# Kernel tuning notes

Hardware: AMD Instinct MI355X
Metric: run time of the kernel (lower is better)

The kernel has to match this reference:

```python
import jax, jax.numpy as jnp
import numpy as np

N_NODES = 50000
N_EDGES = 800000
IN_DIM = 128
HID_DIM = 64
OUT_DIM = 40
N_REL = 8


def setup_inputs() -> dict:
    key = jax.random.key(0)
    ks = jax.random.split(key, 12)
    x = jax.random.normal(ks[0], (N_NODES, IN_DIM), dtype=jnp.float32)
    edge_index = jax.random.randint(ks[1], (2, N_EDGES), 0, N_NODES, dtype=jnp.int64)
    edge_type = jax.random.randint(ks[2], (N_EDGES,), 0, N_REL, dtype=jnp.int64)
    s = 0.05
    W1 = jax.random.normal(ks[3], (N_REL, IN_DIM, HID_DIM), dtype=jnp.float32) * s
    root1 = jax.random.normal(ks[4], (IN_DIM, HID_DIM), dtype=jnp.float32) * s
    b1 = jnp.zeros((HID_DIM,), dtype=jnp.float32)
    W2 = jax.random.normal(ks[5], (N_REL, HID_DIM, HID_DIM), dtype=jnp.float32) * s
    root2 = jax.random.normal(ks[6], (HID_DIM, HID_DIM), dtype=jnp.float32) * s
    b2 = jnp.zeros((HID_DIM,), dtype=jnp.float32)
    Wl = jax.random.normal(ks[7], (HID_DIM, OUT_DIM), dtype=jnp.float32) * s
    bl = jnp.zeros((OUT_DIM,), dtype=jnp.float32)
    return {"x": x, "edge_index": edge_index, "edge_type": edge_type,
            "W1": W1, "root1": root1, "b1": b1,
            "W2": W2, "root2": root2, "b2": b2,
            "Wl": Wl, "bl": bl}


def _rgcn_conv(x, W, Wroot, b, src, dst, edge_type):
    # PyG RGCNConv (no bases/blocks, aggr='mean'):
    #   out[i] = sum_r mean_{(j->i) of rel r} (x[j] @ W[r]) + x[i] @ Wroot + b
    N = x.shape[0]
    R = W.shape[0]
    h = jnp.einsum('ni,rio->rno', x, W)        # [R, N, out]
    msgs = h[edge_type, src]                   # [E, out] edge gather
    seg = edge_type * N + dst                  # per (relation, dst) segment
    sums = jax.ops.segment_sum(msgs, seg, num_segments=R * N)
    cnt = jax.ops.segment_sum(jnp.ones((msgs.shape[0],), x.dtype), seg,
                              num_segments=R * N)
    mean = sums / jnp.maximum(cnt, 1.0)[:, None]
    agg = mean.reshape(R, N, -1).sum(axis=0)   # sum over relations
    return agg + x @ Wroot + b


def reference(x, edge_index, edge_type, W1, root1, b1, W2, root2, b2, Wl, bl):
    src, dst = edge_index[0], edge_index[1]
    h = jax.nn.relu(_rgcn_conv(x, W1, root1, b1, src, dst, edge_type))
    # dropout is identity in eval mode
    h = jax.nn.relu(_rgcn_conv(h, W2, root2, b2, src, dst, edge_type))
    logits = h @ Wl + bl
    return jax.nn.log_softmax(logits, axis=1)
```

## Files before the change

### kernel.cpp

```cpp
#include <hip/hip_runtime.h>
#include <hip/hip_bf16.h>
#include <cmath>


#define IN_DIM 128
#define HID 64
#define OUT_DIM 40
#define NREL 8
#define NCOLS 576
#define K2 576
#define CAPR 32
#define EVR 256
#define CSTR 16

typedef __attribute__((ext_vector_type(8))) short short8;
typedef __attribute__((ext_vector_type(4))) short short4v;
typedef __attribute__((ext_vector_type(4))) float floatx4;

static __device__ __forceinline__ short f2bf(float f) {
  __hip_bfloat16 h = __float2bfloat16(f);
  return __builtin_bit_cast(short, h);
}
static __device__ __forceinline__ float bflo(unsigned int u) {
  return __int_as_float(u << 16);
}
static __device__ __forceinline__ float bfhi(unsigned int u) {
  return __int_as_float(u & 0xffff0000u);
}
static __device__ __forceinline__ unsigned int packbf(float x, float y) {
  unsigned int lo = (unsigned short)f2bf(x);
  unsigned int hi = (unsigned short)f2bf(y);
  return lo | (hi << 16);
}
static __device__ __forceinline__ float bf2f(short s) {
  return __int_as_float(((unsigned int)(unsigned short)s) << 16);
}

__global__ void pack_bt(const float* __restrict__ W1, const float* __restrict__ root1,
                        short* __restrict__ Bt1,
                        const float* __restrict__ W2, const float* __restrict__ root2,
                        short* __restrict__ Bt2b,
                        const float* __restrict__ Wl, short* __restrict__ WlB,
                        int* __restrict__ cursor, int nzero4) {
  const int PB1 = (NCOLS * IN_DIM + 255) / 256;
  const int PB2 = (64 * K2 + 255) / 256;
  const int PBW = (96 * HID + 255) / 256;
  int b = blockIdx.x;
  if (b < PB1) {
    int i = b * 256 + threadIdx.x;
    if (i >= NCOLS * IN_DIM) return;
    int c = i / IN_DIM, k = i % IN_DIM;
    float v = (c < NREL * HID)
      ? W1[((size_t)(c >> 6) * IN_DIM + k) * HID + (c & 63)]
      : root1[(size_t)k * HID + (c - NREL * HID)];
    Bt1[i] = f2bf(v);
  } else if (b < PB1 + PB2) {
    int i = (b - PB1) * 256 + threadIdx.x;
    if (i >= 64 * K2) return;
    int col = i / K2, kk = i % K2;
    float v = (kk < NREL * HID)
      ? W2[(size_t)kk * HID + col]
      : root2[(size_t)(kk - NREL * HID) * HID + col];
    Bt2b[i] = f2bf(v);
  } else if (b < PB1 + PB2 + PBW) {
    int i = (b - PB1 - PB2) * 256 + threadIdx.x;
    if (i >= 96 * HID) return;
    int row = i / HID, k = i % HID;
    int c = row % 48;
    float v = (c < OUT_DIM) ? Wl[(size_t)k * OUT_DIM + c] : 0.f;
    short hi = f2bf(v);
    if (row < 48) WlB[i] = hi;
    else          WlB[i] = f2bf(v - bf2f(hi));
  } else {
    int i = (b - PB1 - PB2 - PBW) * 256 + threadIdx.x;
    if (i < nzero4) {
      int4 z; z.x = 0; z.y = 0; z.z = 0; z.w = 0;
      ((int4*)cursor)[i] = z;
    }
  }
}

__device__ __forceinline__ void gemm1_body(
    short* As, short* Bs,
    const float* __restrict__ A, const short* __restrict__ Bt,
    const float* __restrict__ bias, short* __restrict__ H,
    unsigned short* __restrict__ AGG, int M, int row0)
{
  constexpr int K = IN_DIM;
  constexpr int AST = K + 8;
  int tid = threadIdx.x;
  int wv = tid >> 6, lane = tid & 63;
  int lm = lane & 15, quad = lane >> 4;

  {
    constexpr int CH = K / 4;
    for (int i = tid; i < 64 * CH; i += 256) {
      int r = i / CH, kq = i % CH;
      int gr = row0 + r; if (gr >= M) gr = M - 1;
      float4 v = *(const float4*)(A + (unsigned)(gr * K + kq * 4));
      short4v s;
      s.x = f2bf(v.x); s.y = f2bf(v.y); s.z = f2bf(v.z); s.w = f2bf(v.w);
      *(short4v*)(As + r * AST + kq * 4) = s;
    }
  }

  const short* ap = As + (16 * wv + lm) * AST + quad * 8;

  for (int cy = 0; cy < 9; ++cy) {
    constexpr int CB = K / 8;
    for (int i = tid; i < 64 * CB; i += 256) {
      int n = i / CB, ko = i % CB;
      short8 v = *(const short8*)(Bt + (unsigned)((cy * 64 + n) * K + ko * 8));
      *(short8*)(Bs + n * AST + ko * 8) = v;
    }
    __syncthreads();

    floatx4 acc[4] = {{0,0,0,0},{0,0,0,0},{0,0,0,0},{0,0,0,0}};
    #pragma unroll
    for (int ks = 0; ks < K / 32; ++ks) {
      short8 a = *(const short8*)(ap + ks * 32);
      #pragma unroll
      for (int nb = 0; nb < 4; ++nb) {
        short8 b = *(const short8*)(Bs + (nb * 16 + lm) * AST + ks * 32 + quad * 8);
        acc[nb] = __builtin_amdgcn_mfma_f32_16x16x32_bf16(a, b, acc[nb], 0, 0, 0);
      }
    }
    __syncthreads();

    int mbase = row0 + 16 * wv + quad * 4;
    if (cy < 8) {
      #pragma unroll
      for (int nb = 0; nb < 4; ++nb) {
        int col = cy * 64 + nb * 16 + lm;
        #pragma unroll
        for (int r = 0; r < 4; ++r) {
          int mg = mbase + r;
          if (mg < M) H[(unsigned)mg * (NREL * HID) + col] = f2bf(acc[nb][r]);
        }
      }
    } else {
      #pragma unroll
      for (int nb = 0; nb < 4; ++nb) {
        int col = nb * 16 + lm;
        float bv = bias[col];
        #pragma unroll
        for (int r = 0; r < 4; ++r) {
          int mg = mbase + r;
          if (mg < M)
            AGG[(unsigned)mg * HID + col] = (unsigned short)f2bf(acc[nb][r] + bv);
        }
      }
    }
  }
}

__global__ __launch_bounds__(256, 4) void gemm1_scatter(
    const float* __restrict__ A, const short* __restrict__ Bt,
    const float* __restrict__ bias, short* __restrict__ H,
    unsigned short* __restrict__ AGG, int M, int GB,
    const int* __restrict__ src, const int* __restrict__ dst,
    const int* __restrict__ et,
    int* __restrict__ cursor, int* __restrict__ ev, int E)
{
  constexpr int AST = IN_DIM + 8;
  __shared__ short As[64 * AST];
  __shared__ short Bs[64 * AST];
  if ((int)blockIdx.x < GB) {
    gemm1_body(As, Bs, A, Bt, bias, H, AGG, M, blockIdx.x * 64);
  } else {
    int e = (blockIdx.x - GB) * 256 + threadIdx.x;
    if (e >= E) return;
    int d = dst[e];
    int r = et[e];
    int pos = atomicAdd(&cursor[d * CSTR + r], 1);
    if (pos < CAPR)
      __builtin_nontemporal_store(src[e], &ev[(d << 8) + (r << 5) + pos]);
  }
}

__global__ __launch_bounds__(256) void csr_agg1(
    const short* __restrict__ H1, const int* __restrict__ cursor,
    const int* __restrict__ ev, unsigned short* __restrict__ h, int N)
{
  int tid = threadIdx.x;
  int wv = tid >> 6, lane = tid & 63;
  int rel = lane >> 3, dg = lane & 7;
  int d = blockIdx.x * 4 + wv;

  int cnt = cursor[d * CSTR + rel]; if (cnt > CAPR) cnt = CAPR;
  const int* evg = ev + ((size_t)d << 8) + (rel << 5);
  int evs = evg[dg];

  float acc[8] = {0.f,0.f,0.f,0.f,0.f,0.f,0.f,0.f};
  for (int s = 0; s < cnt; ++s) {
    int srcj = (s < 8) ? __shfl(evs, (lane & 56) + s, 64) : evg[s];
    uint4 hv = *(const uint4*)(H1 + ((size_t)srcj << 9) + (rel << 6) + (dg << 3));
    acc[0] += bflo(hv.x); acc[1] += bfhi(hv.x);
    acc[2] += bflo(hv.y); acc[3] += bfhi(hv.y);
    acc[4] += bflo(hv.z); acc[5] += bfhi(hv.z);
    acc[6] += bflo(hv.w); acc[7] += bfhi(hv.w);
  }
  float w = (cnt > 0) ? (1.0f / (float)cnt) : 0.0f;
  #pragma unroll
  for (int j = 0; j < 8; ++j) acc[j] *= w;
  #pragma unroll
  for (int off = 8; off <= 32; off <<= 1) {
    #pragma unroll
    for (int j = 0; j < 8; ++j) acc[j] += __shfl_xor(acc[j], off, 64);
  }
  if (rel == 0) {
    unsigned short* hrow = h + (size_t)d * HID + (dg << 3);
    uint4 sv = *(const uint4*)hrow;
    float v0 = fmaxf(acc[0] + bflo(sv.x), 0.f);
    float v1 = fmaxf(acc[1] + bfhi(sv.x), 0.f);
    float v2 = fmaxf(acc[2] + bflo(sv.y), 0.f);
    float v3 = fmaxf(acc[3] + bfhi(sv.y), 0.f);
    float v4 = fmaxf(acc[4] + bflo(sv.z), 0.f);
    float v5 = fmaxf(acc[5] + bfhi(sv.z), 0.f);
    float v6 = fmaxf(acc[6] + bflo(sv.w), 0.f);
    float v7 = fmaxf(acc[7] + bfhi(sv.w), 0.f);
    uint4 ov;
    ov.x = packbf(v0, v1); ov.y = packbf(v2, v3);
    ov.z = packbf(v4, v5); ov.w = packbf(v6, v7);
    *(uint4*)hrow = ov;
  }
}

__global__ __launch_bounds__(256) void agg2(
    const unsigned short* __restrict__ h, const int* __restrict__ cursor,
    const int* __restrict__ ev, short* __restrict__ m2, int N)
{
  int tid = threadIdx.x;
  int wv = tid >> 6, lane = tid & 63;
  int rel = lane >> 3, dg = lane & 7;
  int d = blockIdx.x * 4 + wv;

  int cnt = cursor[d * CSTR + rel]; if (cnt > CAPR) cnt = CAPR;
  const int* evg = ev + ((size_t)d << 8) + (rel << 5);
  int evs = evg[dg];

  float acc[8] = {0.f,0.f,0.f,0.f,0.f,0.f,0.f,0.f};
  for (int s = 0; s < cnt; ++s) {
    int srcj = (s < 8) ? __shfl(evs, (lane & 56) + s, 64) : evg[s];
    uint4 hv = *(const uint4*)(h + ((size_t)srcj << 6) + (dg << 3));
    acc[0] += bflo(hv.x); acc[1] += bfhi(hv.x);
    acc[2] += bflo(hv.y); acc[3] += bfhi(hv.y);
    acc[4] += bflo(hv.z); acc[5] += bfhi(hv.z);
    acc[6] += bflo(hv.w); acc[7] += bfhi(hv.w);
  }
  float w = (cnt > 0) ? (1.0f / (float)cnt) : 0.0f;
  uint4 ov;
  ov.x = packbf(acc[0] * w, acc[1] * w);
  ov.y = packbf(acc[2] * w, acc[3] * w);
  ov.z = packbf(acc[4] * w, acc[5] * w);
  ov.w = packbf(acc[6] * w, acc[7] * w);
  *(uint4*)(m2 + (size_t)d * K2 + (rel << 6) + (dg << 3)) = ov;
  if (rel == 0) {
    uint4 hv = *(const uint4*)(h + ((size_t)d << 6) + (dg << 3));
    *(uint4*)(m2 + (size_t)d * K2 + 512 + (dg << 3)) = hv;
  }
}

__global__ __launch_bounds__(256) void gemm2c(
    const short* __restrict__ m2, const short* __restrict__ Bt2b,
    const short* __restrict__ WlB, const float* __restrict__ b2,
    const float* __restrict__ bl, float* __restrict__ out, int N)
{
  constexpr int AST = 64 + 8;
  __shared__ short As[64 * AST];
  __shared__ short Bs[64 * AST];
  __shared__ short zb[64 * AST];
  __shared__ short Wb[96 * AST];
  __shared__ float sb2[64];
  __shared__ float sbl[48];
  int tid = threadIdx.x;
  int wv = tid >> 6, lane = tid & 63;
  int lm = lane & 15, quad = lane >> 4;
  int row0 = blockIdx.x * 64;

  #pragma unroll
  for (int j = 0; j < 3; ++j) {
    int i = tid + j * 256;
    int r = i >> 3, ch = i & 7;
    *(short8*)(Wb + r * AST + ch * 8) = *(const short8*)(WlB + r * 64 + ch * 8);
  }
  if (tid < 64) sb2[tid] = b2[tid];
  if (tid < 48) sbl[tid] = (tid < OUT_DIM) ? bl[tid] : 0.f;

  floatx4 acc[4] = {{0,0,0,0},{0,0,0,0},{0,0,0,0},{0,0,0,0}};
  for (int kt = 0; kt < 9; ++kt) {
    #pragma unroll
    for (int j = 0; j < 2; ++j) {
      int i = tid + j * 256;
      int r = i >> 3, ch = i & 7;
      int gr = row0 + r; if (gr >= N) gr = N - 1;
      *(short8*)(As + r * AST + ch * 8) =
          *(const short8*)(m2 + (size_t)gr * K2 + kt * 64 + ch * 8);
      *(short8*)(Bs + r * AST + ch * 8) =
          *(const short8*)(Bt2b + (unsigned)(r * K2 + kt * 64 + ch * 8));
    }
    __syncthreads();
    #pragma unroll
    for (int ks = 0; ks < 2; ++ks) {
      short8 a = *(const short8*)(As + (16 * wv + lm) * AST + ks * 32 + quad * 8);
      #pragma unroll
      for (int nb = 0; nb < 4; ++nb) {
        short8 b = *(const short8*)(Bs + (nb * 16 + lm) * AST + ks * 32 + quad * 8);
        acc[nb] = __builtin_amdgcn_mfma_f32_16x16x32_bf16(b, a, acc[nb], 0, 0, 0);
      }
    }
    __syncthreads();
  }

  int zrow = 16 * wv + lm;
  #pragma unroll
  for (int nb = 0; nb < 4; ++nb) {
    int c0 = nb * 16 + quad * 4;
    float4 bv = *(const float4*)(sb2 + c0);
    short4v s;
    s.x = f2bf(fmaxf(acc[nb][0] + bv.x, 0.f));
    s.y = f2bf(fmaxf(acc[nb][1] + bv.y, 0.f));
    s.z = f2bf(fmaxf(acc[nb][2] + bv.z, 0.f));
    s.w = f2bf(fmaxf(acc[nb][3] + bv.w, 0.f));
    *(short4v*)(zb + zrow * AST + c0) = s;
  }

  floatx4 acc2[3] = {{0,0,0,0},{0,0,0,0},{0,0,0,0}};
  #pragma unroll
  for (int ks = 0; ks < 2; ++ks) {
    short8 a = *(const short8*)(zb + zrow * AST + ks * 32 + quad * 8);
    #pragma unroll
    for (int nb2 = 0; nb2 < 3; ++nb2) {
      short8 bh = *(const short8*)(Wb + (nb2 * 16 + lm) * AST + ks * 32 + quad * 8);
      short8 bl_ = *(const short8*)(Wb + (48 + nb2 * 16 + lm) * AST + ks * 32 + quad * 8);
      acc2[nb2] = __builtin_amdgcn_mfma_f32_16x16x32_bf16(bh, a, acc2[nb2], 0, 0, 0);
      acc2[nb2] = __builtin_amdgcn_mfma_f32_16x16x32_bf16(bl_, a, acc2[nb2], 0, 0, 0);
    }
  }

  float lv[3][4];
  float m = -__builtin_inff();
  #pragma unroll
  for (int nb2 = 0; nb2 < 3; ++nb2) {
    #pragma unroll
    for (int r = 0; r < 4; ++r) {
      int col = nb2 * 16 + quad * 4 + r;
      float t = acc2[nb2][r] + sbl[col];
      lv[nb2][r] = t;
      if (col < OUT_DIM) m = fmaxf(m, t);
    }
  }
  m = fmaxf(m, __shfl_xor(m, 16, 64));
  m = fmaxf(m, __shfl_xor(m, 32, 64));
  float s = 0.f;
  #pragma unroll
  for (int nb2 = 0; nb2 < 3; ++nb2) {
    #pragma unroll
    for (int r = 0; r < 4; ++r) {
      int col = nb2 * 16 + quad * 4 + r;
      if (col < OUT_DIM) s += expf(lv[nb2][r] - m);
    }
  }
  s += __shfl_xor(s, 16, 64);
  s += __shfl_xor(s, 32, 64);
  float lg = logf(s);
  int dd = row0 + zrow;
  if (dd < N) {
    float* orow = out + (size_t)dd * OUT_DIM;
    #pragma unroll
    for (int nb2 = 0; nb2 < 3; ++nb2) {
      #pragma unroll
      for (int r = 0; r < 4; ++r) {
        int col = nb2 * 16 + quad * 4 + r;
        if (col < OUT_DIM) orow[col] = lv[nb2][r] - m - lg;
      }
    }
  }
}

extern "C" void kernel_launch(void* const* d_in, const int* in_sizes, int n_in,
                              void* d_out, int out_size, void* d_ws, size_t ws_size,
                              hipStream_t stream) {
  const float* x     = (const float*)d_in[0];
  const int*   eidx  = (const int*)d_in[1];
  const int*   etype = (const int*)d_in[2];
  const float* W1    = (const float*)d_in[3];
  const float* root1 = (const float*)d_in[4];
  const float* b1    = (const float*)d_in[5];
  const float* W2    = (const float*)d_in[6];
  const float* root2 = (const float*)d_in[7];
  const float* b2    = (const float*)d_in[8];
  const float* Wl    = (const float*)d_in[9];
  const float* bl    = (const float*)d_in[10];

  int N = in_sizes[0] / IN_DIM;
  int E = in_sizes[2];
  const int* srcp = eidx;
  const int* dstp = eidx + E;

  char* ws = (char*)d_ws;
  size_t off = 0;
  auto alloc = [&](size_t bytes) -> char* {
    char* p = ws + off;
    off += (bytes + 255) & ~(size_t)255;
    return p;
  };
  short* Bt1    = (short*)alloc((size_t)NCOLS * IN_DIM * 2);
  short* Bt2b   = (short*)alloc((size_t)64 * K2 * 2);
  short* WlB    = (short*)alloc((size_t)96 * HID * 2);
  int*   cursor = (int*)alloc((size_t)N * CSTR * 4);
  int*   ev     = (int*)alloc((size_t)N * EVR * 4);
  char*  h1m2   = alloc((size_t)N * K2 * 2);
  short* H1     = (short*)h1m2;
  short* m2     = (short*)h1m2;
  unsigned short* AGG1 = (unsigned short*)alloc((size_t)N * HID * 2);

  const int PB1 = (NCOLS * IN_DIM + 255) / 256;
  const int PB2 = (64 * K2 + 255) / 256;
  const int PBW = (96 * HID + 255) / 256;
  int nzero4 = (N * CSTR) / 4;
  int ZB = (nzero4 + 255) / 256;
  pack_bt<<<PB1 + PB2 + PBW + ZB, 256, 0, stream>>>(
      W1, root1, Bt1, W2, root2, Bt2b, Wl, WlB, cursor, nzero4);

  int GB = (N + 63) / 64;
  int SB = (E + 255) / 256;
  gemm1_scatter<<<GB + SB, 256, 0, stream>>>(x, Bt1, b1, H1, AGG1, N, GB,
                                             srcp, dstp, etype, cursor, ev, E);

  csr_agg1<<<N / 4, 256, 0, stream>>>(H1, cursor, ev, AGG1, N);

  agg2<<<N / 4, 256, 0, stream>>>(AGG1, cursor, ev, m2, N);

  gemm2c<<<GB, 256, 0, stream>>>(m2, Bt2b, WlB, b2, bl, (float*)d_out, N);
}
```

Before: 225.9 us.

## Fuse layer-2 aggregation into GEMM, compact edge buckets, relation-major H1 layout

The agg2 kernel is folded into gemm2c. Each block now gathers and means neighbour features for its 64 rows directly into a full-K shared-memory A tile, so the m2 intermediate no longer makes a round trip through global memory. Edge buckets shrink from 32 slots per relation to 8 inline slots plus a separate spill array, which cuts scatter footprint and lets one coalesced load fetch all 64 indices per node. H1 is stored relation-major and csr_agg1 is rewritten so each lane group handles one edge slot across relations with fixed unrolled loads. The trade-off is a serial spill path for high-degree buckets and much larger shared memory in gemm2c, which may lower occupancy.

Result: slower. 298.8 us (+32.3%).

```diff
diff --git a/kernel.cpp b/kernel.cpp
--- a/kernel.cpp
+++ b/kernel.cpp
@@ -10,7 +10,7 @@
 #define NCOLS 576
 #define K2 576
 #define CAPR 32
-#define EVR 256
+#define SPILLN 24
 #define CSTR 16
 
 typedef __attribute__((ext_vector_type(8))) short short8;
@@ -131,11 +131,12 @@
     if (cy < 8) {
       #pragma unroll
       for (int nb = 0; nb < 4; ++nb) {
-        int col = cy * 64 + nb * 16 + lm;
+        int col = nb * 16 + lm;
         #pragma unroll
         for (int r = 0; r < 4; ++r) {
           int mg = mbase + r;
-          if (mg < M) H[(unsigned)mg * (NREL * HID) + col] = f2bf(acc[nb][r]);
+          if (mg < M)
+            H[(((size_t)cy * M + mg) << 6) + col] = f2bf(acc[nb][r]);
         }
       }
     } else {
@@ -160,7 +161,8 @@
     unsigned short* __restrict__ AGG, int M, int GB,
     const int* __restrict__ src, const int* __restrict__ dst,
     const int* __restrict__ et,
-    int* __restrict__ cursor, int* __restrict__ ev, int E)
+    int* __restrict__ cursor, int* __restrict__ ev8,
+    int* __restrict__ spill, int E)
 {
   constexpr int AST = IN_DIM + 8;
   __shared__ short As[64 * AST];
@@ -173,52 +175,71 @@
     int d = dst[e];
     int r = et[e];
     int pos = atomicAdd(&cursor[d * CSTR + r], 1);
-    if (pos < CAPR)
-      __builtin_nontemporal_store(src[e], &ev[(d << 8) + (r << 5) + pos]);
+    if (pos < 8)
+      __builtin_nontemporal_store(src[e], &ev8[(d << 6) + (r << 3) + pos]);
+    else if (pos < CAPR)
+      __builtin_nontemporal_store(src[e],
+          &spill[((d << 3) + r) * SPILLN + pos - 8]);
   }
 }
 
 __global__ __launch_bounds__(256) void csr_agg1(
-    const short* __restrict__ H1, const int* __restrict__ cursor,
-    const int* __restrict__ ev, unsigned short* __restrict__ h, int N)
+    const short* __restrict__ H1r, const int* __restrict__ cursor,
+    const int* __restrict__ ev8, const int* __restrict__ spill,
+    unsigned short* __restrict__ h, int N)
 {
   int tid = threadIdx.x;
   int wv = tid >> 6, lane = tid & 63;
-  int rel = lane >> 3, dg = lane & 7;
+  int s = lane >> 3, g = lane & 7;
   int d = blockIdx.x * 4 + wv;
 
-  int cnt = cursor[d * CSTR + rel]; if (cnt > CAPR) cnt = CAPR;
-  const int* evg = ev + ((size_t)d << 8) + (rel << 5);
-  int evs = evg[dg];
-
-  float acc[8] = {0.f,0.f,0.f,0.f,0.f,0.f,0.f,0.f};
-  for (int s = 0; s < cnt; ++s) {
-    int srcj = (s < 8) ? __shfl(evs, (lane & 56) + s, 64) : evg[s];
-    uint4 hv = *(const uint4*)(H1 + ((size_t)srcj << 9) + (rel << 6) + (dg << 3));
-    acc[0] += bflo(hv.x); acc[1] += bfhi(hv.x);
-    acc[2] += bflo(hv.y); acc[3] += bfhi(hv.y);
-    acc[4] += bflo(hv.z); acc[5] += bfhi(hv.z);
-    acc[6] += bflo(hv.w); acc[7] += bfhi(hv.w);
-  }
-  float w = (cnt > 0) ? (1.0f / (float)cnt) : 0.0f;
-  #pragma unroll
-  for (int j = 0; j < 8; ++j) acc[j] *= w;
+  int evl = ev8[(d << 6) + lane];
+  const int* crow = cursor + d * CSTR;
+  float pacc[8] = {0.f,0.f,0.f,0.f,0.f,0.f,0.f,0.f};
+
+  #pragma unroll
+  for (int r = 0; r < 8; ++r) {
+    int cnt = crow[r]; if (cnt > CAPR) cnt = CAPR;
+    int cm1 = cnt > 0 ? cnt - 1 : 0;
+    int sc = s < cm1 ? s : cm1;
+    int sv = __shfl(evl, (r << 3) + sc, 64);
+    int srcj = (cnt > 0) ? sv : 0;
+    uint4 hv = *(const uint4*)((const unsigned short*)H1r
+        + (((size_t)r * N + srcj) << 6) + (g << 3));
+    if (s >= cnt) { hv.x = 0u; hv.y = 0u; hv.z = 0u; hv.w = 0u; }
+    float w = (cnt > 0) ? (1.0f / (float)cnt) : 0.0f;
+    pacc[0] += w * bflo(hv.x); pacc[1] += w * bfhi(hv.x);
+    pacc[2] += w * bflo(hv.y); pacc[3] += w * bfhi(hv.y);
+    pacc[4] += w * bflo(hv.z); pacc[5] += w * bfhi(hv.z);
+    pacc[6] += w * bflo(hv.w); pacc[7] += w * bfhi(hv.w);
+    if (cnt > 8 && s == 0) {
+      for (int t = 8; t < cnt; ++t) {
+        int sj = spill[((d << 3) + r) * SPILLN + t - 8];
+        uint4 h2 = *(const uint4*)((const unsigned short*)H1r
+            + (((size_t)r * N + sj) << 6) + (g << 3));
+        pacc[0] += w * bflo(h2.x); pacc[1] += w * bfhi(h2.x);
+        pacc[2] += w * bflo(h2.y); pacc[3] += w * bfhi(h2.y);
+        pacc[4] += w * bflo(h2.z); pacc[5] += w * bfhi(h2.z);
+        pacc[6] += w * bflo(h2.w); pacc[7] += w * bfhi(h2.w);
+      }
+    }
+  }
   #pragma unroll
   for (int off = 8; off <= 32; off <<= 1) {
     #pragma unroll
-    for (int j = 0; j < 8; ++j) acc[j] += __shfl_xor(acc[j], off, 64);
-  }
-  if (rel == 0) {
-    unsigned short* hrow = h + (size_t)d * HID + (dg << 3);
+    for (int j = 0; j < 8; ++j) pacc[j] += __shfl_xor(pacc[j], off, 64);
+  }
+  if (s == 0) {
+    unsigned short* hrow = h + ((size_t)d << 6) + (g << 3);
     uint4 sv = *(const uint4*)hrow;
-    float v0 = fmaxf(acc[0] + bflo(sv.x), 0.f);
-    float v1 = fmaxf(acc[1] + bfhi(sv.x), 0.f);
-    float v2 = fmaxf(acc[2] + bflo(sv.y), 0.f);
-    float v3 = fmaxf(acc[3] + bfhi(sv.y), 0.f);
-    float v4 = fmaxf(acc[4] + bflo(sv.z), 0.f);
-    float v5 = fmaxf(acc[5] + bfhi(sv.z), 0.f);
-    float v6 = fmaxf(acc[6] + bflo(sv.w), 0.f);
-    float v7 = fmaxf(acc[7] + bfhi(sv.w), 0.f);
+    float v0 = fmaxf(pacc[0] + bflo(sv.x), 0.f);
+    float v1 = fmaxf(pacc[1] + bfhi(sv.x), 0.f);
+    float v2 = fmaxf(pacc[2] + bflo(sv.y), 0.f);
+    float v3 = fmaxf(pacc[3] + bfhi(sv.y), 0.f);
+    float v4 = fmaxf(pacc[4] + bflo(sv.z), 0.f);
+    float v5 = fmaxf(pacc[5] + bfhi(sv.z), 0.f);
+    float v6 = fmaxf(pacc[6] + bflo(sv.w), 0.f);
+    float v7 = fmaxf(pacc[7] + bfhi(sv.w), 0.f);
     uint4 ov;
     ov.x = packbf(v0, v1); ov.y = packbf(v2, v3);
     ov.z = packbf(v4, v5); ov.w = packbf(v6, v7);
@@ -226,48 +247,16 @@
   }
 }
 
-__global__ __launch_bounds__(256) void agg2(
+__global__ __launch_bounds__(256) void gemm2c(
     const unsigned short* __restrict__ h, const int* __restrict__ cursor,
-    const int* __restrict__ ev, short* __restrict__ m2, int N)
-{
-  int tid = threadIdx.x;
-  int wv = tid >> 6, lane = tid & 63;
-  int rel = lane >> 3, dg = lane & 7;
-  int d = blockIdx.x * 4 + wv;
-
-  int cnt = cursor[d * CSTR + rel]; if (cnt > CAPR) cnt = CAPR;
-  const int* evg = ev + ((size_t)d << 8) + (rel << 5);
-  int evs = evg[dg];
-
-  float acc[8] = {0.f,0.f,0.f,0.f,0.f,0.f,0.f,0.f};
-  for (int s = 0; s < cnt; ++s) {
-    int srcj = (s < 8) ? __shfl(evs, (lane & 56) + s, 64) : evg[s];
-    uint4 hv = *(const uint4*)(h + ((size_t)srcj << 6) + (dg << 3));
-    acc[0] += bflo(hv.x); acc[1] += bfhi(hv.x);
-    acc[2] += bflo(hv.y); acc[3] += bfhi(hv.y);
-    acc[4] += bflo(hv.z); acc[5] += bfhi(hv.z);
-    acc[6] += bflo(hv.w); acc[7] += bfhi(hv.w);
-  }
-  float w = (cnt > 0) ? (1.0f / (float)cnt) : 0.0f;
-  uint4 ov;
-  ov.x = packbf(acc[0] * w, acc[1] * w);
-  ov.y = packbf(acc[2] * w, acc[3] * w);
-  ov.z = packbf(acc[4] * w, acc[5] * w);
-  ov.w = packbf(acc[6] * w, acc[7] * w);
-  *(uint4*)(m2 + (size_t)d * K2 + (rel << 6) + (dg << 3)) = ov;
-  if (rel == 0) {
-    uint4 hv = *(const uint4*)(h + ((size_t)d << 6) + (dg << 3));
-    *(uint4*)(m2 + (size_t)d * K2 + 512 + (dg << 3)) = hv;
-  }
-}
-
-__global__ __launch_bounds__(256) void gemm2c(
-    const short* __restrict__ m2, const short* __restrict__ Bt2b,
-    const short* __restrict__ WlB, const float* __restrict__ b2,
-    const float* __restrict__ bl, float* __restrict__ out, int N)
+    const int* __restrict__ ev8, const int* __restrict__ spill,
+    const short* __restrict__ Bt2b, const short* __restrict__ WlB,
+    const float* __restrict__ b2, const float* __restrict__ bl,
+    float* __restrict__ out, int N)
 {
   constexpr int AST = 64 + 8;
-  __shared__ short As[64 * AST];
+  constexpr int ASTA = K2 + 8;
+  __shared__ short As[64 * ASTA];
   __shared__ short Bs[64 * AST];
   __shared__ short zb[64 * AST];
   __shared__ short Wb[96 * AST];
@@ -276,6 +265,7 @@
   int tid = threadIdx.x;
   int wv = tid >> 6, lane = tid & 63;
   int lm = lane & 15, quad = lane >> 4;
+  int rel = lane >> 3, g = lane & 7;
   int row0 = blockIdx.x * 64;
 
   #pragma unroll
@@ -287,22 +277,61 @@
   if (tid < 64) sb2[tid] = b2[tid];
   if (tid < 48) sbl[tid] = (tid < OUT_DIM) ? bl[tid] : 0.f;
 
+  for (int it = 0; it < 16; ++it) {
+    int dloc = wv * 16 + it;
+    int d = row0 + dloc; if (d >= N) d = N - 1;
+    int evl = ev8[(d << 6) + lane];
+    int cnt = cursor[d * CSTR + rel]; if (cnt > CAPR) cnt = CAPR;
+    int cm1 = cnt > 0 ? cnt - 1 : 0;
+    float a0 = 0.f, a1 = 0.f, a2 = 0.f, a3 = 0.f;
+    float a4 = 0.f, a5 = 0.f, a6 = 0.f, a7 = 0.f;
+    #pragma unroll
+    for (int ss = 0; ss < 8; ++ss) {
+      int sc = ss < cm1 ? ss : cm1;
+      int sv = __shfl(evl, (rel << 3) + sc, 64);
+      int srcj = (cnt > 0) ? sv : 0;
+      uint4 hv = *(const uint4*)(h + ((size_t)srcj << 6) + (g << 3));
+      if (ss >= cnt) { hv.x = 0u; hv.y = 0u; hv.z = 0u; hv.w = 0u; }
+      a0 += bflo(hv.x); a1 += bfhi(hv.x);
+      a2 += bflo(hv.y); a3 += bfhi(hv.y);
+      a4 += bflo(hv.z); a5 += bfhi(hv.z);
+      a6 += bflo(hv.w); a7 += bfhi(hv.w);
+    }
+    if (cnt > 8) {
+      for (int t = 8; t < cnt; ++t) {
+        int sj = spill[((d << 3) + rel) * SPILLN + t - 8];
+        uint4 hv = *(const uint4*)(h + ((size_t)sj << 6) + (g << 3));
+        a0 += bflo(hv.x); a1 += bfhi(hv.x);
+        a2 += bflo(hv.y); a3 += bfhi(hv.y);
+        a4 += bflo(hv.z); a5 += bfhi(hv.z);
+        a6 += bflo(hv.w); a7 += bfhi(hv.w);
+      }
+    }
+    float w = (cnt > 0) ? (1.0f / (float)cnt) : 0.0f;
+    uint4 ov;
+    ov.x = packbf(a0 * w, a1 * w); ov.y = packbf(a2 * w, a3 * w);
+    ov.z = packbf(a4 * w, a5 * w); ov.w = packbf(a6 * w, a7 * w);
+    *(uint4*)(As + dloc * ASTA + (rel << 6) + (g << 3)) = ov;
+    if (rel == 0) {
+      uint4 hv = *(const uint4*)(h + ((size_t)d << 6) + (g << 3));
+      *(uint4*)(As + dloc * ASTA + 512 + (g << 3)) = hv;
+    }
+  }
+
   floatx4 acc[4] = {{0,0,0,0},{0,0,0,0},{0,0,0,0},{0,0,0,0}};
   for (int kt = 0; kt < 9; ++kt) {
     #pragma unroll
     for (int j = 0; j < 2; ++j) {
       int i = tid + j * 256;
       int r = i >> 3, ch = i & 7;
-      int gr = row0 + r; if (gr >= N) gr = N - 1;
-      *(short8*)(As + r * AST + ch * 8) =
-          *(const short8*)(m2 + (size_t)gr * K2 + kt * 64 + ch * 8);
       *(short8*)(Bs + r * AST + ch * 8) =
           *(const short8*)(Bt2b + (unsigned)(r * K2 + kt * 64 + ch * 8));
     }
     __syncthreads();
     #pragma unroll
     for (int ks = 0; ks < 2; ++ks) {
-      short8 a = *(const short8*)(As + (16 * wv + lm) * AST + ks * 32 + quad * 8);
+      short8 a = *(const short8*)(As + (16 * wv + lm) * ASTA + kt * 64
+                                  + ks * 32 + quad * 8);
       #pragma unroll
       for (int nb = 0; nb < 4; ++nb) {
         short8 b = *(const short8*)(Bs + (nb * 16 + lm) * AST + ks * 32 + quad * 8);
@@ -409,11 +438,10 @@
   short* Bt2b   = (short*)alloc((size_t)64 * K2 * 2);
   short* WlB    = (short*)alloc((size_t)96 * HID * 2);
   int*   cursor = (int*)alloc((size_t)N * CSTR * 4);
-  int*   ev     = (int*)alloc((size_t)N * EVR * 4);
-  char*  h1m2   = alloc((size_t)N * K2 * 2);
-  short* H1     = (short*)h1m2;
-  short* m2     = (short*)h1m2;
-  unsigned short* AGG1 = (unsigned short*)alloc((size_t)N * HID * 2);
+  int*   ev8    = (int*)alloc((size_t)N * 64 * 4);
+  int*   spill  = (int*)alloc((size_t)N * NREL * SPILLN * 4);
+  short* H1r    = (short*)alloc((size_t)NREL * N * HID * 2);
+  unsigned short* h = (unsigned short*)alloc((size_t)N * HID * 2);
 
   const int PB1 = (NCOLS * IN_DIM + 255) / 256;
   const int PB2 = (64 * K2 + 255) / 256;
@@ -425,12 +453,12 @@
 
   int GB = (N + 63) / 64;
   int SB = (E + 255) / 256;
-  gemm1_scatter<<<GB + SB, 256, 0, stream>>>(x, Bt1, b1, H1, AGG1, N, GB,
-                                             srcp, dstp, etype, cursor, ev, E);
-
-  csr_agg1<<<N / 4, 256, 0, stream>>>(H1, cursor, ev, AGG1, N);
-
-  agg2<<<N / 4, 256, 0, stream>>>(AGG1, cursor, ev, m2, N);
-
-  gemm2c<<<GB, 256, 0, stream>>>(m2, Bt2b, WlB, b2, bl, (float*)d_out, N);
-}
+  gemm1_scatter<<<GB + SB, 256, 0, stream>>>(x, Bt1, b1, H1r, h, N, GB,
+                                             srcp, dstp, etype,
+                                             cursor, ev8, spill, E);
+
+  csr_agg1<<<N / 4, 256, 0, stream>>>(H1r, cursor, ev8, spill, h, N);
+
+  gemm2c<<<GB, 256, 0, stream>>>(h, cursor, ev8, spill, Bt2b, WlB,
+                                 b2, bl, (float*)d_out, N);
+}
```
